# Kernel optimization log

Hardware: AMD Instinct MI355X
Metric: run time of the kernel (lower is better)

The kernel has to match this reference:

```python
import jax, jax.numpy as jnp
import numpy as np

TWO_PI = 2.0 * np.pi
INV_4PI = 1.0 / (4.0 * np.pi)


def _net(xc, B_rff, W1, b1, W2, b2, W3, b3, W4, b4, W5, b5):
    # Random Fourier features: [N,3] @ [3,1024] -> sin/cos concat -> [N,2048]
    proj = TWO_PI * (xc @ B_rff)
    y = jnp.concatenate([jnp.sin(proj), jnp.cos(proj)], axis=-1)
    h = jax.nn.softplus(y @ W1 + b1)
    h = jax.nn.softplus(h @ W2 + b2)
    h = jax.nn.softplus(h @ W3 + b3)
    h = jax.nn.softplus(h @ W4 + b4)
    return h @ W5 + b5  # [N,1]


def _biot_savart(x, bdry):
    # x: [b,N,3]; bdry: [b,L,M,3] closed loops sampled at M points.
    seg = jnp.roll(bdry, -1, axis=2) - bdry           # segment tangents [b,L,M,3]
    mid = 0.5 * (jnp.roll(bdry, -1, axis=2) + bdry)   # segment midpoints [b,L,M,3]
    diff = x[:, :, None, None, :] - mid[:, None]      # [b,N,L,M,3]
    num = jnp.cross(jnp.broadcast_to(seg[:, None], diff.shape), diff)
    r3 = jnp.sum(diff * diff, axis=-1, keepdims=True) ** 1.5
    return INV_4PI * jnp.sum(num / r3, axis=(2, 3))   # [b,N,3]


def setup_inputs() -> dict:
    key = jax.random.key(0)
    ks = jax.random.split(key, 8)
    N, M, SIGMA = 65536, 512, 2.0
    x = jax.random.uniform(ks[0], (N, 3), jnp.float32, -1.0, 1.0)
    # boundary: one closed loop (circle of radius 0.8 in the z=0 plane)
    t = jnp.linspace(0.0, TWO_PI, M, endpoint=False)
    circ = jnp.stack([jnp.cos(t), jnp.sin(t), jnp.zeros_like(t)], axis=-1)
    bdry = (0.8 * circ)[None, None].astype(jnp.float32)  # [1,1,M,3]
    B_rff = jax.random.normal(ks[1], (3, 1024), jnp.float32) * SIGMA

    def lin(k, fi, fo):
        kw, kb = jax.random.split(k)
        lim = 1.0 / np.sqrt(fi)
        W = jax.random.uniform(kw, (fi, fo), jnp.float32, -lim, lim)
        b = jax.random.uniform(kb, (fo,), jnp.float32, -lim, lim)
        return W, b

    W1, b1 = lin(ks[2], 2048, 256)
    W2, b2 = lin(ks[3], 256, 256)
    W3, b3 = lin(ks[4], 256, 256)
    W4, b4 = lin(ks[5], 256, 256)
    W5, b5 = lin(ks[6], 256, 1)
    return dict(x=x, bdry=bdry, B_rff=B_rff, W1=W1, b1=b1, W2=W2, b2=b2,
                W3=W3, b3=b3, W4=W4, b4=b4, W5=W5, b5=b5)


def reference(x, bdry, B_rff, W1, b1, W2, b2, W3, b3, W4, b4, W5, b5):
    xc = jnp.clip(x, -1.0, 1.0)
    net = lambda p: _net(p, B_rff, W1, b1, W2, b2, W3, b3, W4, b4, W5, b5)
    f = net(xc)                                            # [N,1]
    # df/dx: f_i depends only on x_i, so grad of the sum is the per-point grad
    df = jax.grad(lambda p: net(p).sum())(xc)              # [N,3]
    alpha = _biot_savart(xc.reshape(bdry.shape[0], -1, 3), bdry)  # [1,N,3]
    current = df + alpha.reshape(-1, 3)
    return f, current, df, alpha
```

## Files before the change

### kernel.cpp

```cpp
#include <hip/hip_runtime.h>
#include <math.h>
#include <stdint.h>

typedef __bf16 bf16x8 __attribute__((ext_vector_type(8)));
typedef float f32x4 __attribute__((ext_vector_type(4)));
typedef unsigned int uint4v __attribute__((ext_vector_type(4)));

#define TWO_PI_F 6.28318530717958647692f
#define INV_4PI_F 0.079577471545947667884f

#define NPHASE 176
#define S_W2F 524288
#define S_W1B 917504
#define PACK_CHUNKS_TOTAL 180224
#define PACK_BLOCKS 176
#define H_OFF 1441792ll
#define H_STRIDE 16777216ll

typedef __attribute__((address_space(1))) const unsigned int GU32;
typedef __attribute__((address_space(3))) unsigned int LU32;
__device__ __forceinline__ void gll16(const __bf16* g, __bf16* l) {
  __builtin_amdgcn_global_load_lds((GU32*)(uintptr_t)(const void*)g,
                                   (LU32*)(unsigned int)(uintptr_t)(void*)l,
                                   16, 0, 0);
}

__device__ __forceinline__ float sin2pi(float t) {
  return __builtin_amdgcn_sinf(__builtin_amdgcn_fractf(t));
}
__device__ __forceinline__ float cos2pi(float t) {
  return __builtin_amdgcn_cosf(__builtin_amdgcn_fractf(t));
}

__launch_bounds__(1024)
__global__ void k_prep(const float* __restrict__ W1, const float* __restrict__ W2,
                       const float* __restrict__ W3, const float* __restrict__ W4,
                       const float* __restrict__ x, const float* __restrict__ bdry,
                       float* __restrict__ out, __bf16* __restrict__ ws,
                       int N, int M) {
  __shared__ float se[512 * 3];
  __shared__ float sm[512 * 3];
  __shared__ float red[3 * 256 * 3];

  if (blockIdx.x < PACK_BLOCKS) {
    int gid = blockIdx.x * 1024 + threadIdx.x;
    if (gid >= PACK_CHUNKS_TOTAL) return;
    const float* W; int n, q, ct, kc; bool bwd; long dstoff;
    if (gid < 65536) {
      int c = gid; n = c & 15; q = (c >> 4) & 3; ct = (c >> 6) & 15; kc = c >> 10;
      W = W1; bwd = false; dstoff = (long)c * 8;
    } else if (gid < 131072) {
      int c = gid - 65536; n = c & 15; q = (c >> 4) & 3; kc = (c >> 6) & 7; ct = c >> 9;
      int newct = ((ct & 63) << 1) | (ct >> 6);
      long newc = (((long)newct * 8 + kc) * 4 + q) * 16 + n;
      W = W1; bwd = true; dstoff = S_W1B + newc * 8;
    } else {
      int g = gid - 131072; int r = g >> 13; int c = g & 8191;
      n = c & 15; q = (c >> 4) & 3; ct = (c >> 6) & 15; kc = c >> 10;
      W = (r < 2) ? W2 : (r < 4) ? W3 : W4; bwd = (r & 1);
      int layer = r >> 1;
      int newr = bwd ? (5 - layer) : layer;
      dstoff = S_W2F + (long)newr * 65536 + (long)c * 8;
    }
    int k0 = kc * 32 + q * 8;
    int ngl = ct * 16 + n;
    bf16x8 v;
    #pragma unroll
    for (int j = 0; j < 8; ++j) {
      float f = bwd ? W[ngl * 256 + (k0 + j)] : W[(k0 + j) * 256 + ngl];
      v[j] = (__bf16)f;
    }
    *(bf16x8*)(ws + dstoff) = v;
    return;
  }

  const int tid = threadIdx.x;
  for (int s = tid; s < M; s += 1024) {
    int sn = (s + 1 == M) ? 0 : s + 1;
    float b0 = bdry[s * 3 + 0], b1 = bdry[s * 3 + 1], b2 = bdry[s * 3 + 2];
    float c0 = bdry[sn * 3 + 0], c1 = bdry[sn * 3 + 1], c2 = bdry[sn * 3 + 2];
    se[s * 3 + 0] = c0 - b0; se[s * 3 + 1] = c1 - b1; se[s * 3 + 2] = c2 - b2;
    sm[s * 3 + 0] = 0.5f * (c0 + b0);
    sm[s * 3 + 1] = 0.5f * (c1 + b1);
    sm[s * 3 + 2] = 0.5f * (c2 + b2);
  }
  __syncthreads();
  const int p = tid & 255;
  const int q = tid >> 8;
  const int idx = (blockIdx.x - PACK_BLOCKS) * 256 + p;
  float x0 = fminf(fmaxf(x[idx * 3 + 0], -1.f), 1.f);
  float x1 = fminf(fmaxf(x[idx * 3 + 1], -1.f), 1.f);
  float x2 = fminf(fmaxf(x[idx * 3 + 2], -1.f), 1.f);
  const int mq = M >> 2;
  float a0 = 0.f, a1 = 0.f, a2 = 0.f;
  #pragma unroll 4
  for (int it = 0; it < mq; ++it) {
    int s = q * mq + it;
    float e0 = se[s * 3 + 0], e1 = se[s * 3 + 1], e2 = se[s * 3 + 2];
    float d0 = x0 - sm[s * 3 + 0], d1 = x1 - sm[s * 3 + 1], d2 = x2 - sm[s * 3 + 2];
    float r2 = d0 * d0 + d1 * d1 + d2 * d2;
    float inv = rsqrtf(r2);
    float inv3 = inv * inv * inv;
    float n0 = e1 * d2 - e2 * d1;
    float n1 = e2 * d0 - e0 * d2;
    float n2 = e0 * d1 - e1 * d0;
    a0 = fmaf(n0, inv3, a0); a1 = fmaf(n1, inv3, a1); a2 = fmaf(n2, inv3, a2);
  }
  if (q) {
    float* rp = &red[((q - 1) * 256 + p) * 3];
    rp[0] = a0; rp[1] = a1; rp[2] = a2;
  }
  __syncthreads();
  if (q == 0) {
    #pragma unroll
    for (int c = 0; c < 3; ++c) {
      const float* rp = &red[(c * 256 + p) * 3];
      a0 += rp[0]; a1 += rp[1]; a2 += rp[2];
    }
    float* alpha = out + (size_t)7 * N;
    alpha[idx * 3 + 0] = a0 * INV_4PI_F;
    alpha[idx * 3 + 1] = a1 * INV_4PI_F;
    alpha[idx * 3 + 2] = a2 * INV_4PI_F;
  }
}

template <int NT>
__launch_bounds__(256, 2)
__global__ void k_mlp(const float* __restrict__ x, const float* __restrict__ Brff,
                      const float* __restrict__ b1, const float* __restrict__ b2,
                      const float* __restrict__ b3, const float* __restrict__ b4,
                      const float* __restrict__ W5, const float* __restrict__ b5,
                      const __bf16* __restrict__ wsw, __bf16* __restrict__ hstash,
                      float* __restrict__ out, int N) {
  __shared__ __attribute__((aligned(16))) __bf16 sW[2][8192];
  __shared__ __attribute__((aligned(16))) __bf16 sConv[16384];
  __shared__ __attribute__((aligned(16))) float  sBr[3072];

  const int tid  = threadIdx.x;
  const int wave = tid >> 6;
  const int lane = tid & 63;
  const int ml   = lane & 15;
  const int quad = lane >> 4;
  const int rowbase = blockIdx.x * (64 * NT) + wave * (16 * NT);
  const int gw = blockIdx.x * 4 + wave;

  __bf16* conv = sConv + wave * 4096;

  auto ISSUE = [&](int t) {
    if (t >= NPHASE) return;
    const __bf16* src = wsw + (size_t)t * 8192;
    __bf16* dst = &sW[t & 1][0];
    #pragma unroll
    for (int r = 0; r < 4; ++r) {
      int idx = tid + r * 256;
      gll16(src + (size_t)idx * 8, dst + idx * 8);
    }
  };

  float4 bt0 = ((const float4*)Brff)[tid];
  float4 bt1 = ((const float4*)Brff)[tid + 256];
  float4 bt2 = ((const float4*)Brff)[tid + 512];

  float xa[NT][3];
  #pragma unroll
  for (int t = 0; t < NT; ++t) {
    const float* xp = x + (size_t)(rowbase + t * 16 + ml) * 3;
    #pragma unroll
    for (int i = 0; i < 3; ++i) xa[t][i] = fminf(fmaxf(xp[i], -1.f), 1.f);
  }

  ISSUE(0);
  ((float4*)sBr)[tid]       = bt0;
  ((float4*)sBr)[tid + 256] = bt1;
  ((float4*)sBr)[tid + 512] = bt2;

  f32x4 acc[NT][16];
  bf16x8 afr[NT][8];
  bf16x8 h1f[8], h2f[8], h3f[8];

  auto zero_acc = [&]() {
    #pragma unroll
    for (int t = 0; t < NT; ++t)
      #pragma unroll
      for (int ct = 0; ct < 16; ++ct) { f32x4 z = {0.f, 0.f, 0.f, 0.f}; acc[t][ct] = z; }
  };
  auto conv_widx = [&](int ct, int r) -> int {
    return (((ct >> 1) * 4 + ((ct & 1) << 1) + (ml >> 3)) * 16 + quad * 4 + r) * 8 + (ml & 7);
  };

  __syncthreads();

  zero_acc();
  for (int kc = 0; kc < 64; ++kc) {
    ISSUE(kc + 1);
    int cb = (kc * 32 + quad * 8) & 1023;
    bool issin = (kc < 32);
    bf16x8 af[NT];
    #pragma unroll
    for (int j = 0; j < 8; ++j) {
      float w0 = sBr[cb + j], w1 = sBr[1024 + cb + j], w2 = sBr[2048 + cb + j];
      #pragma unroll
      for (int t = 0; t < NT; ++t) {
        float tt = xa[t][0] * w0 + xa[t][1] * w1 + xa[t][2] * w2;
        af[t][j] = (__bf16)(issin ? sin2pi(tt) : cos2pi(tt));
      }
    }
    const __bf16* wb = &sW[kc & 1][0];
    #pragma unroll
    for (int ct = 0; ct < 16; ++ct) {
      bf16x8 bfr = *(const bf16x8*)(wb + (ct * 4 + quad) * 128 + ml * 8);
      #pragma unroll
      for (int t = 0; t < NT; ++t)
        acc[t][ct] = __builtin_amdgcn_mfma_f32_16x16x32_bf16(af[t], bfr, acc[t][ct], 0, 0, 0);
    }
    __syncthreads();
  }

  auto epilogue_h = [&](const float* __restrict__ bias, bf16x8* keep, int l) {
    #pragma unroll
    for (int t = 0; t < NT; ++t) {
      #pragma unroll
      for (int ct = 0; ct < 16; ++ct) {
        float bcol = bias[ct * 16 + ml];
        #pragma unroll
        for (int r = 0; r < 4; ++r) {
          float z = acc[t][ct][r] + bcol;
          float h = fmaxf(z, 0.f) + __logf(1.f + __expf(-fabsf(z)));
          conv[conv_widx(ct, r)] = (__bf16)h;
        }
      }
      #pragma unroll
      for (int ks = 0; ks < 8; ++ks)
        afr[t][ks] = *(const bf16x8*)(conv + (ks * 4 + quad) * 128 + ml * 8);
      if constexpr (NT == 2) {
        __bf16* hp = hstash + (size_t)l * H_STRIDE + (size_t)(gw * 2 + t) * 4096 + lane * 8;
        #pragma unroll
        for (int ks = 0; ks < 8; ++ks)
          *(bf16x8*)(hp + ks * 512) = afr[t][ks];
      }
    }
    if constexpr (NT == 1) {
      #pragma unroll
      for (int ks = 0; ks < 8; ++ks) keep[ks] = afr[0][ks];
    }
  };

  auto gemm256 = [&](int t0) {
    zero_acc();
    #pragma unroll
    for (int kc = 0; kc < 8; ++kc) {
      ISSUE(t0 + kc + 1);
      const __bf16* wb = &sW[(t0 + kc) & 1][0];
      #pragma unroll
      for (int ct = 0; ct < 16; ++ct) {
        bf16x8 bfr = *(const bf16x8*)(wb + (ct * 4 + quad) * 128 + ml * 8);
        #pragma unroll
        for (int t = 0; t < NT; ++t)
          acc[t][ct] = __builtin_amdgcn_mfma_f32_16x16x32_bf16(afr[t][kc], bfr, acc[t][ct], 0, 0, 0);
      }
      __syncthreads();
    }
  };

  epilogue_h(b1, h1f, 0);
  gemm256(64);
  epilogue_h(b2, h2f, 1);
  gemm256(72);
  epilogue_h(b3, h3f, 2);
  gemm256(80);

  {
    float fpart[NT][4];
    #pragma unroll
    for (int t = 0; t < NT; ++t)
      #pragma unroll
      for (int r = 0; r < 4; ++r) fpart[t][r] = 0.f;
    #pragma unroll
    for (int t = 0; t < NT; ++t) {
      #pragma unroll
      for (int ct = 0; ct < 16; ++ct) {
        float bcol = b4[ct * 16 + ml];
        float w5   = W5[ct * 16 + ml];
        #pragma unroll
        for (int r = 0; r < 4; ++r) {
          float z = acc[t][ct][r] + bcol;
          float ez = __expf(-fabsf(z));
          float sp = fmaxf(z, 0.f) + __logf(1.f + ez);
          float sig = (z >= 0.f) ? 1.f / (1.f + ez) : ez / (1.f + ez);
          fpart[t][r] += sp * w5;
          conv[conv_widx(ct, r)] = (__bf16)(sig * w5);
        }
      }
      #pragma unroll
      for (int r = 0; r < 4; ++r) {
        float v = fpart[t][r];
        #pragma unroll
        for (int m = 1; m < 16; m <<= 1) v += __shfl_xor(v, m, 64);
        if (ml == 0) out[rowbase + t * 16 + quad * 4 + r] = v + b5[0];
      }
      #pragma unroll
      for (int ks = 0; ks < 8; ++ks)
        afr[t][ks] = *(const bf16x8*)(conv + (ks * 4 + quad) * 128 + ml * 8);
    }
  }

  auto epilogue_g = [&](const bf16x8* keep, int l) {
    #pragma unroll
    for (int t = 0; t < NT; ++t) {
      bf16x8 hv[8];
      if constexpr (NT == 2) {
        const __bf16* hp = hstash + (size_t)l * H_STRIDE + (size_t)(gw * 2 + t) * 4096 + lane * 8;
        #pragma unroll
        for (int ks = 0; ks < 8; ++ks) hv[ks] = *(const bf16x8*)(hp + ks * 512);
      }
      #pragma unroll
      for (int ct = 0; ct < 16; ++ct)
        #pragma unroll
        for (int r = 0; r < 4; ++r) conv[conv_widx(ct, r)] = (__bf16)acc[t][ct][r];
      #pragma unroll
      for (int ks = 0; ks < 8; ++ks) {
        bf16x8 g = *(const bf16x8*)(conv + (ks * 4 + quad) * 128 + ml * 8);
        bf16x8 o;
        #pragma unroll
        for (int j = 0; j < 8; ++j) {
          float gp = (float)g[j];
          float h  = (NT == 2) ? (float)hv[ks][j] : (float)keep[ks][j];
          o[j] = (__bf16)(gp * (1.f - __expf(-h)));
        }
        afr[t][ks] = o;
      }
    }
  };

  gemm256(88);  epilogue_g(h3f, 2);
  gemm256(96);  epilogue_g(h2f, 1);
  gemm256(104); epilogue_g(h1f, 0);

  float xr[NT][4][3];
  #pragma unroll
  for (int t = 0; t < NT; ++t)
    #pragma unroll
    for (int r = 0; r < 4; ++r) {
      const float* xp = x + (size_t)(rowbase + t * 16 + quad * 4 + r) * 3;
      #pragma unroll
      for (int i = 0; i < 3; ++i) xr[t][r][i] = fminf(fmaxf(xp[i], -1.f), 1.f);
    }
  float dxa[NT][4][3];
  #pragma unroll
  for (int t = 0; t < NT; ++t)
    #pragma unroll
    for (int r = 0; r < 4; ++r) { dxa[t][r][0] = 0.f; dxa[t][r][1] = 0.f; dxa[t][r][2] = 0.f; }

  for (int p = 0; p < 64; ++p) {
    int tp = 112 + p;
    ISSUE(tp + 1);
    const __bf16* wb = &sW[tp & 1][0];
    f32x4 aA[NT], aB[NT];
    #pragma unroll
    for (int t = 0; t < NT; ++t) {
      f32x4 z = {0.f, 0.f, 0.f, 0.f}; aA[t] = z; aB[t] = z;
    }
    #pragma unroll
    for (int ks = 0; ks < 8; ++ks) {
      bf16x8 bA = *(const bf16x8*)(wb + (ks * 4 + quad) * 128 + ml * 8);
      bf16x8 bB = *(const bf16x8*)(wb + 4096 + (ks * 4 + quad) * 128 + ml * 8);
      #pragma unroll
      for (int t = 0; t < NT; ++t) {
        aA[t] = __builtin_amdgcn_mfma_f32_16x16x32_bf16(afr[t][ks], bA, aA[t], 0, 0, 0);
        aB[t] = __builtin_amdgcn_mfma_f32_16x16x32_bf16(afr[t][ks], bB, aB[t], 0, 0, 0);
      }
    }
    int c = p * 16 + ml;
    float B0 = sBr[c], B1 = sBr[1024 + c], B2 = sBr[2048 + c];
    #pragma unroll
    for (int t = 0; t < NT; ++t) {
      #pragma unroll
      for (int r = 0; r < 4; ++r) {
        float tt = xr[t][r][0] * B0 + xr[t][r][1] * B1 + xr[t][r][2] * B2;
        float tf = __builtin_amdgcn_fractf(tt);
        float sn = __builtin_amdgcn_sinf(tf);
        float cs = __builtin_amdgcn_cosf(tf);
        float dp = aA[t][r] * cs - aB[t][r] * sn;
        dxa[t][r][0] = fmaf(dp, B0, dxa[t][r][0]);
        dxa[t][r][1] = fmaf(dp, B1, dxa[t][r][1]);
        dxa[t][r][2] = fmaf(dp, B2, dxa[t][r][2]);
      }
    }
    __syncthreads();
  }

  #pragma unroll
  for (int t = 0; t < NT; ++t)
    #pragma unroll
    for (int r = 0; r < 4; ++r)
      #pragma unroll
      for (int i = 0; i < 3; ++i) {
        float v = dxa[t][r][i] * TWO_PI_F;
        #pragma unroll
        for (int m = 1; m < 16; m <<= 1) v += __shfl_xor(v, m, 64);
        if (ml == 0) {
          int row = rowbase + t * 16 + quad * 4 + r;
          out[(size_t)4 * N + row * 3 + i] = v;
          out[(size_t)N + row * 3 + i] = v + out[(size_t)7 * N + row * 3 + i];
        }
      }
}

extern "C" void kernel_launch(void* const* d_in, const int* in_sizes, int n_in,
                              void* d_out, int out_size, void* d_ws, size_t ws_size,
                              hipStream_t stream) {
  const float* x    = (const float*)d_in[0];
  const float* bdry = (const float*)d_in[1];
  const float* Brff = (const float*)d_in[2];
  const float* W1   = (const float*)d_in[3];
  const float* b1   = (const float*)d_in[4];
  const float* W2   = (const float*)d_in[5];
  const float* b2   = (const float*)d_in[6];
  const float* W3   = (const float*)d_in[7];
  const float* b3   = (const float*)d_in[8];
  const float* W4   = (const float*)d_in[9];
  const float* b4   = (const float*)d_in[10];
  const float* W5   = (const float*)d_in[11];
  const float* b5   = (const float*)d_in[12];
  float* out = (float*)d_out;
  __bf16* ws = (__bf16*)d_ws;
  int N = in_sizes[0] / 3;
  int M = in_sizes[1] / 3;

  k_prep<<<PACK_BLOCKS + N / 256, 1024, 0, stream>>>(W1, W2, W3, W4, x, bdry, out, ws, N, M);

  size_t need = (size_t)(H_OFF + 3 * H_STRIDE) * sizeof(__bf16);
  if (ws_size >= need) {
    k_mlp<2><<<N / 128, 256, 0, stream>>>(x, Brff, b1, b2, b3, b4, W5, b5,
                                          ws, ws + H_OFF, out, N);
  } else {
    k_mlp<1><<<N / 64, 256, 0, stream>>>(x, Brff, b1, b2, b3, b4, W5, b5,
                                         ws, nullptr, out, N);
  }
}
```

Measured before the change: 357.6 us.

## Fuse Biot-Savart into MLP kernel and interleave sin/cos feature columns

Moves the Biot-Savart boundary integral out of the prep kernel and into the tail of the MLP kernel. Each block stages the boundary points in shared memory, splits segments across thread groups, and writes alpha and current together, so current no longer reads alpha back from global memory. W1 rows are repacked so each RFF phase yields an interleaved sin/cos pair from one fract, which halves the phase dot products in the first layer. The cost is extra per-block tail work and shared-memory reuse inside the MLP kernel, and segment tangents and midpoints are now recomputed per point instead of precomputed.

```diff
diff --git a/kernel.cpp b/kernel.cpp
--- a/kernel.cpp
+++ b/kernel.cpp
@@ -4,7 +4,6 @@
 
 typedef __bf16 bf16x8 __attribute__((ext_vector_type(8)));
 typedef float f32x4 __attribute__((ext_vector_type(4)));
-typedef unsigned int uint4v __attribute__((ext_vector_type(4)));
 
 #define TWO_PI_F 6.28318530717958647692f
 #define INV_4PI_F 0.079577471545947667884f
@@ -25,113 +24,53 @@
                                    16, 0, 0);
 }
 
-__device__ __forceinline__ float sin2pi(float t) {
-  return __builtin_amdgcn_sinf(__builtin_amdgcn_fractf(t));
-}
-__device__ __forceinline__ float cos2pi(float t) {
-  return __builtin_amdgcn_cosf(__builtin_amdgcn_fractf(t));
-}
-
 __launch_bounds__(1024)
 __global__ void k_prep(const float* __restrict__ W1, const float* __restrict__ W2,
                        const float* __restrict__ W3, const float* __restrict__ W4,
-                       const float* __restrict__ x, const float* __restrict__ bdry,
-                       float* __restrict__ out, __bf16* __restrict__ ws,
-                       int N, int M) {
-  __shared__ float se[512 * 3];
-  __shared__ float sm[512 * 3];
-  __shared__ float red[3 * 256 * 3];
-
-  if (blockIdx.x < PACK_BLOCKS) {
-    int gid = blockIdx.x * 1024 + threadIdx.x;
-    if (gid >= PACK_CHUNKS_TOTAL) return;
-    const float* W; int n, q, ct, kc; bool bwd; long dstoff;
-    if (gid < 65536) {
-      int c = gid; n = c & 15; q = (c >> 4) & 3; ct = (c >> 6) & 15; kc = c >> 10;
-      W = W1; bwd = false; dstoff = (long)c * 8;
-    } else if (gid < 131072) {
-      int c = gid - 65536; n = c & 15; q = (c >> 4) & 3; kc = (c >> 6) & 7; ct = c >> 9;
-      int newct = ((ct & 63) << 1) | (ct >> 6);
-      long newc = (((long)newct * 8 + kc) * 4 + q) * 16 + n;
-      W = W1; bwd = true; dstoff = S_W1B + newc * 8;
-    } else {
-      int g = gid - 131072; int r = g >> 13; int c = g & 8191;
-      n = c & 15; q = (c >> 4) & 3; ct = (c >> 6) & 15; kc = c >> 10;
-      W = (r < 2) ? W2 : (r < 4) ? W3 : W4; bwd = (r & 1);
-      int layer = r >> 1;
-      int newr = bwd ? (5 - layer) : layer;
-      dstoff = S_W2F + (long)newr * 65536 + (long)c * 8;
-    }
-    int k0 = kc * 32 + q * 8;
-    int ngl = ct * 16 + n;
-    bf16x8 v;
-    #pragma unroll
-    for (int j = 0; j < 8; ++j) {
-      float f = bwd ? W[ngl * 256 + (k0 + j)] : W[(k0 + j) * 256 + ngl];
-      v[j] = (__bf16)f;
-    }
-    *(bf16x8*)(ws + dstoff) = v;
-    return;
-  }
-
-  const int tid = threadIdx.x;
-  for (int s = tid; s < M; s += 1024) {
-    int sn = (s + 1 == M) ? 0 : s + 1;
-    float b0 = bdry[s * 3 + 0], b1 = bdry[s * 3 + 1], b2 = bdry[s * 3 + 2];
-    float c0 = bdry[sn * 3 + 0], c1 = bdry[sn * 3 + 1], c2 = bdry[sn * 3 + 2];
-    se[s * 3 + 0] = c0 - b0; se[s * 3 + 1] = c1 - b1; se[s * 3 + 2] = c2 - b2;
-    sm[s * 3 + 0] = 0.5f * (c0 + b0);
-    sm[s * 3 + 1] = 0.5f * (c1 + b1);
-    sm[s * 3 + 2] = 0.5f * (c2 + b2);
-  }
-  __syncthreads();
-  const int p = tid & 255;
-  const int q = tid >> 8;
-  const int idx = (blockIdx.x - PACK_BLOCKS) * 256 + p;
-  float x0 = fminf(fmaxf(x[idx * 3 + 0], -1.f), 1.f);
-  float x1 = fminf(fmaxf(x[idx * 3 + 1], -1.f), 1.f);
-  float x2 = fminf(fmaxf(x[idx * 3 + 2], -1.f), 1.f);
-  const int mq = M >> 2;
-  float a0 = 0.f, a1 = 0.f, a2 = 0.f;
-  #pragma unroll 4
-  for (int it = 0; it < mq; ++it) {
-    int s = q * mq + it;
-    float e0 = se[s * 3 + 0], e1 = se[s * 3 + 1], e2 = se[s * 3 + 2];
-    float d0 = x0 - sm[s * 3 + 0], d1 = x1 - sm[s * 3 + 1], d2 = x2 - sm[s * 3 + 2];
-    float r2 = d0 * d0 + d1 * d1 + d2 * d2;
-    float inv = rsqrtf(r2);
-    float inv3 = inv * inv * inv;
-    float n0 = e1 * d2 - e2 * d1;
-    float n1 = e2 * d0 - e0 * d2;
-    float n2 = e0 * d1 - e1 * d0;
-    a0 = fmaf(n0, inv3, a0); a1 = fmaf(n1, inv3, a1); a2 = fmaf(n2, inv3, a2);
-  }
-  if (q) {
-    float* rp = &red[((q - 1) * 256 + p) * 3];
-    rp[0] = a0; rp[1] = a1; rp[2] = a2;
-  }
-  __syncthreads();
-  if (q == 0) {
-    #pragma unroll
-    for (int c = 0; c < 3; ++c) {
-      const float* rp = &red[(c * 256 + p) * 3];
-      a0 += rp[0]; a1 += rp[1]; a2 += rp[2];
-    }
-    float* alpha = out + (size_t)7 * N;
-    alpha[idx * 3 + 0] = a0 * INV_4PI_F;
-    alpha[idx * 3 + 1] = a1 * INV_4PI_F;
-    alpha[idx * 3 + 2] = a2 * INV_4PI_F;
-  }
+                       __bf16* __restrict__ ws) {
+  int gid = blockIdx.x * 1024 + threadIdx.x;
+  if (gid >= PACK_CHUNKS_TOTAL) return;
+  const float* W; int n, q, ct, kc; bool bwd; long dstoff;
+  bool w1f = false;
+  if (gid < 65536) {
+    int c = gid; n = c & 15; q = (c >> 4) & 3; ct = (c >> 6) & 15; kc = c >> 10;
+    W = W1; bwd = false; w1f = true; dstoff = (long)c * 8;
+  } else if (gid < 131072) {
+    int c = gid - 65536; n = c & 15; q = (c >> 4) & 3; kc = (c >> 6) & 7; ct = c >> 9;
+    int newct = ((ct & 63) << 1) | (ct >> 6);
+    long newc = (((long)newct * 8 + kc) * 4 + q) * 16 + n;
+    W = W1; bwd = true; dstoff = S_W1B + newc * 8;
+  } else {
+    int g = gid - 131072; int r = g >> 13; int c = g & 8191;
+    n = c & 15; q = (c >> 4) & 3; ct = (c >> 6) & 15; kc = c >> 10;
+    W = (r < 2) ? W2 : (r < 4) ? W3 : W4; bwd = (r & 1);
+    int layer = r >> 1;
+    int newr = bwd ? (5 - layer) : layer;
+    dstoff = S_W2F + (long)newr * 65536 + (long)c * 8;
+  }
+  int k0 = kc * 32 + q * 8;
+  int ngl = ct * 16 + n;
+  bf16x8 v;
+  #pragma unroll
+  for (int j = 0; j < 8; ++j) {
+    int kg = k0 + j;
+    int row = w1f ? ((kg & 1) ? 1024 + (kg >> 1) : (kg >> 1)) : kg;
+    float f = bwd ? W[ngl * 256 + (kg + 0)] : W[row * 256 + ngl];
+    if (bwd) f = W[ngl * 256 + kg];
+    v[j] = (__bf16)f;
+  }
+  *(bf16x8*)(ws + dstoff) = v;
 }
 
 template <int NT>
 __launch_bounds__(256, 2)
 __global__ void k_mlp(const float* __restrict__ x, const float* __restrict__ Brff,
+                      const float* __restrict__ bdry,
                       const float* __restrict__ b1, const float* __restrict__ b2,
                       const float* __restrict__ b3, const float* __restrict__ b4,
                       const float* __restrict__ W5, const float* __restrict__ b5,
                       const __bf16* __restrict__ wsw, __bf16* __restrict__ hstash,
-                      float* __restrict__ out, int N) {
+                      float* __restrict__ out, int N, int M) {
   __shared__ __attribute__((aligned(16))) __bf16 sW[2][8192];
   __shared__ __attribute__((aligned(16))) __bf16 sConv[16384];
   __shared__ __attribute__((aligned(16))) float  sBr[3072];
@@ -141,7 +80,8 @@
   const int lane = tid & 63;
   const int ml   = lane & 15;
   const int quad = lane >> 4;
-  const int rowbase = blockIdx.x * (64 * NT) + wave * (16 * NT);
+  const int ROWS = 64 * NT;
+  const int rowbase = blockIdx.x * ROWS + wave * (16 * NT);
   const int gw = blockIdx.x * 4 + wave;
 
   __bf16* conv = sConv + wave * 4096;
@@ -193,16 +133,18 @@
   zero_acc();
   for (int kc = 0; kc < 64; ++kc) {
     ISSUE(kc + 1);
-    int cb = (kc * 32 + quad * 8) & 1023;
-    bool issin = (kc < 32);
+    int cb = kc * 16 + quad * 4;
     bf16x8 af[NT];
     #pragma unroll
-    for (int j = 0; j < 8; ++j) {
-      float w0 = sBr[cb + j], w1 = sBr[1024 + cb + j], w2 = sBr[2048 + cb + j];
+    for (int i = 0; i < 4; ++i) {
+      int c = cb + i;
+      float w0 = sBr[c], w1 = sBr[1024 + c], w2 = sBr[2048 + c];
       #pragma unroll
       for (int t = 0; t < NT; ++t) {
         float tt = xa[t][0] * w0 + xa[t][1] * w1 + xa[t][2] * w2;
-        af[t][j] = (__bf16)(issin ? sin2pi(tt) : cos2pi(tt));
+        float tf = __builtin_amdgcn_fractf(tt);
+        af[t][2 * i]     = (__bf16)__builtin_amdgcn_sinf(tf);
+        af[t][2 * i + 1] = (__bf16)__builtin_amdgcn_cosf(tf);
       }
     }
     const __bf16* wb = &sW[kc & 1][0];
@@ -389,6 +331,7 @@
     __syncthreads();
   }
 
+  float* dfsave = (float*)sConv + 1024;
   #pragma unroll
   for (int t = 0; t < NT; ++t)
     #pragma unroll
@@ -399,11 +342,66 @@
         #pragma unroll
         for (int m = 1; m < 16; m <<= 1) v += __shfl_xor(v, m, 64);
         if (ml == 0) {
-          int row = rowbase + t * 16 + quad * 4 + r;
-          out[(size_t)4 * N + row * 3 + i] = v;
-          out[(size_t)N + row * 3 + i] = v + out[(size_t)7 * N + row * 3 + i];
+          int lrow = wave * (16 * NT) + t * 16 + quad * 4 + r;
+          out[(size_t)4 * N + (size_t)(blockIdx.x * ROWS + lrow) * 3 + i] = v;
+          dfsave[lrow * 3 + i] = v;
         }
       }
+
+  {
+    float* sb = (float*)sW;
+    for (int i = tid; i < M * 3; i += 256) sb[i] = bdry[i];
+    __syncthreads();
+
+    const int GRP = 256 / ROWS;
+    const int segs = M / GRP;
+    int pt = tid % ROWS, g = tid / ROWS;
+    int row = blockIdx.x * ROWS + pt;
+    const float* xp = x + (size_t)row * 3;
+    float x0 = fminf(fmaxf(xp[0], -1.f), 1.f);
+    float x1 = fminf(fmaxf(xp[1], -1.f), 1.f);
+    float x2 = fminf(fmaxf(xp[2], -1.f), 1.f);
+    float a0 = 0.f, a1 = 0.f, a2 = 0.f;
+    for (int it = 0; it < segs; ++it) {
+      int s = g * segs + it;
+      int s1 = (s + 1 == M) ? 0 : s + 1;
+      float b0 = sb[s * 3 + 0], b1v = sb[s * 3 + 1], b2v = sb[s * 3 + 2];
+      float c0 = sb[s1 * 3 + 0], c1 = sb[s1 * 3 + 1], c2 = sb[s1 * 3 + 2];
+      float e0 = c0 - b0, e1 = c1 - b1v, e2 = c2 - b2v;
+      float d0 = x0 - 0.5f * (c0 + b0);
+      float d1 = x1 - 0.5f * (c1 + b1v);
+      float d2 = x2 - 0.5f * (c2 + b2v);
+      float r2 = d0 * d0 + d1 * d1 + d2 * d2;
+      float inv = rsqrtf(r2);
+      float inv3 = inv * inv * inv;
+      float n0 = e1 * d2 - e2 * d1;
+      float n1 = e2 * d0 - e0 * d2;
+      float n2 = e0 * d1 - e1 * d0;
+      a0 = fmaf(n0, inv3, a0); a1 = fmaf(n1, inv3, a1); a2 = fmaf(n2, inv3, a2);
+    }
+    float* red = (float*)sConv;
+    if (g) {
+      float* rp = red + ((g - 1) * ROWS + pt) * 3;
+      rp[0] = a0; rp[1] = a1; rp[2] = a2;
+    }
+    __syncthreads();
+    if (g == 0) {
+      #pragma unroll 4
+      for (int q = 0; q < GRP - 1; ++q) {
+        const float* rp = red + (q * ROWS + pt) * 3;
+        a0 += rp[0]; a1 += rp[1]; a2 += rp[2];
+      }
+      a0 *= INV_4PI_F; a1 *= INV_4PI_F; a2 *= INV_4PI_F;
+      float* alpha = out + (size_t)7 * N;
+      alpha[(size_t)row * 3 + 0] = a0;
+      alpha[(size_t)row * 3 + 1] = a1;
+      alpha[(size_t)row * 3 + 2] = a2;
+      const float* dfp = dfsave + pt * 3;
+      out[(size_t)N + (size_t)row * 3 + 0] = dfp[0] + a0;
+      out[(size_t)N + (size_t)row * 3 + 1] = dfp[1] + a1;
+      out[(size_t)N + (size_t)row * 3 + 2] = dfp[2] + a2;
+    }
+  }
 }
 
 extern "C" void kernel_launch(void* const* d_in, const int* in_sizes, int n_in,
@@ -427,14 +425,14 @@
   int N = in_sizes[0] / 3;
   int M = in_sizes[1] / 3;
 
-  k_prep<<<PACK_BLOCKS + N / 256, 1024, 0, stream>>>(W1, W2, W3, W4, x, bdry, out, ws, N, M);
+  k_prep<<<PACK_BLOCKS, 1024, 0, stream>>>(W1, W2, W3, W4, ws);
 
   size_t need = (size_t)(H_OFF + 3 * H_STRIDE) * sizeof(__bf16);
   if (ws_size >= need) {
-    k_mlp<2><<<N / 128, 256, 0, stream>>>(x, Brff, b1, b2, b3, b4, W5, b5,
-                                          ws, ws + H_OFF, out, N);
+    k_mlp<2><<<N / 128, 256, 0, stream>>>(x, Brff, bdry, b1, b2, b3, b4, W5, b5,
+                                          ws, ws + H_OFF, out, N, M);
   } else {
-    k_mlp<1><<<N / 64, 256, 0, stream>>>(x, Brff, b1, b2, b3, b4, W5, b5,
-                                         ws, nullptr, out, N);
+    k_mlp<1><<<N / 64, 256, 0, stream>>>(x, Brff, bdry, b1, b2, b3, b4, W5, b5,
+                                         ws, nullptr, out, N, M);
   }
 }
```

New measurement: 330.4 us. 1.08x faster.
